# Performance work log

Measured on AMD Instinct MI355X. Metric: run time of the kernel, lower is better.

The kernel has to match this reference:

```python
import jax, jax.numpy as jnp
import numpy as np

H = 512      # cfg.hidden_size
I = 512      # input_size
T = 64       # cfg.recurrence
B = 1024     # num_trajectories

def setup_inputs() -> dict:
    key = jax.random.key(0)
    ks = jax.random.split(key, 7)
    s = 1.0 / np.sqrt(H)
    head_output = jax.random.normal(ks[0], (B * T, I), jnp.float32)
    rnn_states = jax.random.normal(ks[1], (B, 2 * H), jnp.float32)
    dones = jax.random.randint(ks[2], (B * T,), 0, 2).astype(jnp.float32)
    W_ih = jax.random.uniform(ks[3], (4 * H, I), jnp.float32, -s, s)
    W_hh = jax.random.uniform(ks[4], (4 * H, H), jnp.float32, -s, s)
    b_ih = jax.random.uniform(ks[5], (4 * H,), jnp.float32, -s, s)
    b_hh = jax.random.uniform(ks[6], (4 * H,), jnp.float32, -s, s)
    return {"head_output": head_output, "rnn_states": rnn_states, "dones": dones,
            "W_ih": W_ih, "W_hh": W_hh, "b_ih": b_ih, "b_hh": b_hh}

def reference(head_output, rnn_states, dones, W_ih, W_hh, b_ih, b_hh):
    # h, c: [B, H] each (num_layers == 1)
    h0, c0 = jnp.split(rnn_states, 2, axis=1)
    x_seq = head_output.reshape(B, T, I).transpose(1, 0, 2)  # [T, B, I]
    # is_new_episode = dones rolled by 1 along time, first step forced to 0
    d = dones.reshape(B, T)
    is_new = jnp.roll(d, 1, axis=1).at[:, 0].set(0.0)  # [B, T]
    masks = is_new.T  # [T, B]
    # precompute input projection for all steps (same math, hoisted out of the loop)
    x_proj = jnp.einsum('tbi,gi->tbg', x_seq, W_ih) + b_ih + b_hh  # [T, B, 4H]

    def step(carry, inp):
        h, c = carry
        xp, m = inp
        keep = (1.0 - m)[:, None]  # zero state at episode boundaries
        h = h * keep
        c = c * keep
        gates = xp + h @ W_hh.T  # [B, 4H], torch gate order i,f,g,o
        i_g, f_g, g_g, o_g = jnp.split(gates, 4, axis=1)
        i_g = jax.nn.sigmoid(i_g)
        f_g = jax.nn.sigmoid(f_g)
        g_g = jnp.tanh(g_g)
        o_g = jax.nn.sigmoid(o_g)
        c = f_g * c + i_g * g_g
        h = o_g * jnp.tanh(c)
        return (h, c), (h, c)

    (hT, cT), (hs, cs) = jax.lax.scan(step, (h0, c0), (x_proj, masks))
    # outputs at each step are h (output of single-layer LSTM)
    x = hs.transpose(1, 0, 2).reshape(B * T, H)  # [B*T, H]
    new_rnn_states = jnp.concatenate((hT, cT), axis=1)  # [B, 2H]
    h_stack = hs[:, None, :, :]  # [T, 1, B, H] (num_layers dim)
    c_stack = cs[:, None, :, :]
    return x, new_rnn_states, (h_stack, c_stack)
```

## Files before the change

kernel.cpp:

```cpp
#include <hip/hip_runtime.h>
#include <stdint.h>


#define WC_OFF   0u
#define HF_OFF   4194304u
#define CF_OFF   5242880u
#define BIAS_OFF 7340032u
#define F_WIH   0u
#define F_WHH   2097152u
#define F_HF    4194304u
#define F_CF    5242880u
#define F_BIAS  7340032u
#define F_XBF   8388608u
#define F_XPROJ 75497472u
#define F_NEED  343932928u
#define OUT_RNN  33554432u
#define OUT_HS   34603008u
#define OUT_CS   68157440u

typedef __attribute__((ext_vector_type(4))) float f32x4;
typedef __attribute__((ext_vector_type(8))) short s16x8;
typedef __attribute__((ext_vector_type(4))) unsigned int u32x4;
typedef __attribute__((ext_vector_type(4))) unsigned short u16x4;

__device__ __forceinline__ unsigned short f2bf(float f) {
  union { float f; unsigned int u; } v; v.f = f;
  return (unsigned short)((v.u + 0x7FFFu + ((v.u >> 16) & 1u)) >> 16);
}
__device__ __forceinline__ float bf2f(unsigned short s) {
  union { unsigned int u; float f; } v; v.u = ((unsigned int)s) << 16;
  return v.f;
}
__device__ __forceinline__ unsigned int pack2(float a, float b) {
  return (unsigned int)f2bf(a) | ((unsigned int)f2bf(b) << 16);
}
__device__ __forceinline__ float sigm(float x) { return 1.0f / (1.0f + __expf(-x)); }

__device__ __forceinline__ void gl_lds16(const void* g, void* lds) {
  __builtin_amdgcn_global_load_lds(
      (const __attribute__((address_space(1))) unsigned int*)g,
      (__attribute__((address_space(3))) unsigned int*)lds, 16, 0, 0);
}



__global__ void __launch_bounds__(256) prep_fast(
    const float* __restrict__ xg, const float* __restrict__ rnn,
    const float* __restrict__ Wih, const float* __restrict__ Whh,
    const float* __restrict__ bih, const float* __restrict__ bhh,
    unsigned char* __restrict__ ws) {
  unsigned int tid = blockIdx.x * 256u + threadIdx.x;
  unsigned short* wih_f = (unsigned short*)(ws + F_WIH);
  unsigned short* whh_f = (unsigned short*)(ws + F_WHH);
  unsigned short* hf    = (unsigned short*)(ws + F_HF);
  float* cf   = (float*)(ws + F_CF);
  float* bias = (float*)(ws + F_BIAS);
  unsigned short* xbf = (unsigned short*)(ws + F_XBF);
  if (tid < 131072u) {
    unsigned int frag = tid >> 6, l = tid & 63u;
    unsigned int cb = frag >> 4, ks = frag & 15u;
    unsigned int g  = cb * 16u + (l & 15u);
    unsigned int k0 = ks * 32u + ((l >> 4) << 3);
    const float* src = Wih + (size_t)g * 512u + k0;
    u32x4 p;
    p.x = pack2(src[0], src[1]); p.y = pack2(src[2], src[3]);
    p.z = pack2(src[4], src[5]); p.w = pack2(src[6], src[7]);
    *(u32x4*)(wih_f + (size_t)frag * 512u + l * 8u) = p;
  } else if (tid < 262144u) {
    unsigned int t2 = tid - 131072u;
    unsigned int frag = t2 >> 6, l = t2 & 63u;
    unsigned int cb = frag >> 4, ks = frag & 15u;
    unsigned int g  = cb * 16u + (l & 15u);
    unsigned int k0 = ks * 32u + ((l >> 4) << 3);
    const float* src = Whh + (size_t)g * 512u + k0;
    u32x4 p;
    p.x = pack2(src[0], src[1]); p.y = pack2(src[2], src[3]);
    p.z = pack2(src[4], src[5]); p.w = pack2(src[6], src[7]);
    *(u32x4*)(whh_f + (size_t)frag * 512u + l * 8u) = p;
  } else if (tid < 327680u) {
    unsigned int t2 = tid - 262144u;
    unsigned int frag = t2 >> 6, l = t2 & 63u;
    unsigned int mb = frag >> 4, ks = frag & 15u;
    unsigned int b  = mb * 16u + (l & 15u);
    unsigned int c0 = ks * 32u + ((l >> 4) << 3);
    const float* src = rnn + (size_t)b * 1024u + c0;
    u32x4 p;
    p.x = pack2(src[0], src[1]); p.y = pack2(src[2], src[3]);
    p.z = pack2(src[4], src[5]); p.w = pack2(src[6], src[7]);
    *(u32x4*)(hf + (size_t)frag * 512u + l * 8u) = p;
  } else if (tid < 458752u) {
    unsigned int t2 = tid - 327680u;
    unsigned int frag = t2 >> 6, l = t2 & 63u;
    unsigned int mb = frag >> 5, cfi = frag & 31u;
    unsigned int hcol = cfi * 16u + (l & 15u);
    f32x4 p;
    #pragma unroll
    for (int r = 0; r < 4; ++r) {
      unsigned int b = mb * 16u + ((l >> 4) << 2) + r;
      p[r] = rnn[(size_t)b * 1024u + 512u + hcol];
    }
    *(f32x4*)(cf + (size_t)frag * 256u + l * 4u) = p;
  } else if (tid < 460800u) {
    unsigned int g = tid - 458752u;
    bias[g] = bih[g] + bhh[g];
  } else if (tid < 4655104u) {
    unsigned int t2 = tid - 460800u;
    unsigned int frag = t2 >> 6, l = t2 & 63u;
    unsigned int ks = frag & 15u, mb = (frag >> 4) & 63u, t = frag >> 10;
    unsigned int b  = mb * 16u + (l & 15u);
    unsigned int k0 = ks * 32u + ((l >> 4) << 3);
    const float* src = xg + ((size_t)(b * 64u + t)) * 512u + k0;
    u32x4 p;
    p.x = pack2(src[0], src[1]); p.y = pack2(src[2], src[3]);
    p.z = pack2(src[4], src[5]); p.w = pack2(src[6], src[7]);
    *(u32x4*)(xbf + (size_t)frag * 512u + l * 8u) = p;
  }
}

__global__ void __launch_bounds__(256) gemm_xproj(unsigned char* __restrict__ ws) {
  const unsigned short* xbf = (const unsigned short*)(ws + F_XBF);
  const unsigned short* wih = (const unsigned short*)(ws + F_WIH);
  const float* bias = (const float*)(ws + F_BIAS);
  unsigned short* xproj = (unsigned short*)(ws + F_XPROJ);

  __shared__ __align__(16) unsigned char smem[65536];
  const int tid = threadIdx.x;
  const int w = tid >> 6, l = tid & 63;
  const int mh = w & 1, nh = w >> 1;
  const int bid = blockIdx.x;
  const int t = bid >> 7, mtile = (bid >> 4) & 7, ntile = bid & 15;

  f32x4 acc[4][4];
  {
    f32x4 z = {0.f, 0.f, 0.f, 0.f};
    #pragma unroll
    for (int i = 0; i < 4; ++i)
      #pragma unroll
      for (int j = 0; j < 4; ++j) acc[i][j] = z;
  }

  auto stage = [&](int kc, int buf) {
    unsigned char* ab = smem + buf * 16384;
    unsigned char* bb = smem + 32768 + buf * 16384;
    #pragma unroll
    for (int j = 0; j < 4; ++j) {
      int idx = w * 4 + j;
      int mb_l = idx >> 1, ksl = idx & 1;
      size_t frag = (size_t)(t * 64 + mtile * 8 + mb_l) * 16u + kc * 2 + ksl;
      gl_lds16(xbf + (frag * 64u + l) * 8u, ab + idx * 1024);
    }
    #pragma unroll
    for (int j = 0; j < 4; ++j) {
      int idx = w * 4 + j;
      int cb_l = idx >> 1, ksl = idx & 1;
      size_t frag = (size_t)(ntile * 8 + cb_l) * 16u + kc * 2 + ksl;
      gl_lds16(wih + (frag * 64u + l) * 8u, bb + idx * 1024);
    }
  };

  stage(0, 0);
  __syncthreads();
  for (int kc = 0; kc < 8; ++kc) {
    int cur = kc & 1;
    if (kc < 7) stage(kc + 1, cur ^ 1);
    unsigned char* ab = smem + cur * 16384;
    unsigned char* bb = smem + 32768 + cur * 16384;
    s16x8 afr[4][2], bfr[4][2];
    #pragma unroll
    for (int m = 0; m < 4; ++m)
      #pragma unroll
      for (int ksl = 0; ksl < 2; ++ksl)
        afr[m][ksl] = *(const s16x8*)(ab + ((mh * 4 + m) * 2 + ksl) * 1024 + l * 16);
    #pragma unroll
    for (int n = 0; n < 4; ++n)
      #pragma unroll
      for (int ksl = 0; ksl < 2; ++ksl)
        bfr[n][ksl] = *(const s16x8*)(bb + ((nh * 4 + n) * 2 + ksl) * 1024 + l * 16);
    #pragma unroll
    for (int m = 0; m < 4; ++m)
      #pragma unroll
      for (int n = 0; n < 4; ++n)
        #pragma unroll
        for (int ksl = 0; ksl < 2; ++ksl)
          acc[m][n] = __builtin_amdgcn_mfma_f32_16x16x32_bf16(
              afr[m][ksl], bfr[n][ksl], acc[m][n], 0, 0, 0);
    __syncthreads();
  }

  #pragma unroll
  for (int m = 0; m < 4; ++m) {
    int mb_abs = mtile * 8 + mh * 4 + m;
    #pragma unroll
    for (int n = 0; n < 4; ++n) {
      int n_abs = ntile * 8 + nh * 4 + n;
      float bc = bias[n_abs * 16 + (l & 15)];
      u16x4 p;
      #pragma unroll
      for (int r = 0; r < 4; ++r) p[r] = f2bf(acc[m][n][r] + bc);
      *(u16x4*)(xproj + ((size_t)(t * 64 + mb_abs) * 128u + n_abs) * 256u + l * 4u) = p;
    }
  }
}

__global__ void __launch_bounds__(256) step_fast(
    const float* __restrict__ dones, unsigned char* __restrict__ ws,
    float* __restrict__ out, int t) {
  const unsigned short* whh = (const unsigned short*)(ws + F_WHH);
  unsigned short* hf = (unsigned short*)(ws + F_HF);
  float* cf = (float*)(ws + F_CF);
  const unsigned short* xproj = (const unsigned short*)(ws + F_XPROJ);

  __shared__ __align__(16) unsigned char smem[49152];
  const int tid = threadIdx.x;
  const int w = tid >> 6, l = tid & 63;
  const int mh = w & 1, ch = w >> 1;
  const int mt = (int)blockIdx.x >> 4, ht = (int)blockIdx.x & 15;

  f32x4 acc[2][4];
  {
    f32x4 z = {0.f, 0.f, 0.f, 0.f};
    #pragma unroll
    for (int i = 0; i < 2; ++i)
      #pragma unroll
      for (int j = 0; j < 4; ++j) acc[i][j] = z;
  }

  auto stage = [&](int kc, int buf) {
    unsigned char* bb = smem + 16384 + buf * 16384;
    #pragma unroll
    for (int j = 0; j < 4; ++j) {
      int idx = w * 4 + j;
      int g = idx >> 2, cbl = (idx >> 1) & 1, ksl = idx & 1;
      int cb = g * 32 + ht * 2 + cbl;
      int ks = kc * 2 + ksl;
      gl_lds16(whh + ((size_t)(cb * 16 + ks) * 64u + l) * 8u, bb + idx * 1024);
    }
    unsigned char* ab = smem + buf * 8192;
    #pragma unroll
    for (int j = 0; j < 2; ++j) {
      int idx = w * 2 + j;
      int mb_l = idx >> 1, ksl = idx & 1;
      int frag = (mt * 4 + mb_l) * 16 + kc * 2 + ksl;
      gl_lds16(hf + ((size_t)frag * 64u + l) * 8u, ab + idx * 1024);
    }
  };

  stage(0, 0);
  __syncthreads();
  for (int kc = 0; kc < 8; ++kc) {
    int cur = kc & 1;
    if (kc < 7) stage(kc + 1, cur ^ 1);
    unsigned char* ab = smem + cur * 8192;
    unsigned char* bb = smem + 16384 + cur * 16384;
    s16x8 afr[2][2], bfr[4][2];
    #pragma unroll
    for (int mb2 = 0; mb2 < 2; ++mb2)
      #pragma unroll
      for (int ksl = 0; ksl < 2; ++ksl)
        afr[mb2][ksl] = *(const s16x8*)(ab + ((mh * 2 + mb2) * 2 + ksl) * 1024 + l * 16);
    #pragma unroll
    for (int g = 0; g < 4; ++g)
      #pragma unroll
      for (int ksl = 0; ksl < 2; ++ksl)
        bfr[g][ksl] = *(const s16x8*)(bb + (g * 4 + ch * 2 + ksl) * 1024 + l * 16);
    #pragma unroll
    for (int mb2 = 0; mb2 < 2; ++mb2)
      #pragma unroll
      for (int g = 0; g < 4; ++g)
        #pragma unroll
        for (int ksl = 0; ksl < 2; ++ksl)
          acc[mb2][g] = __builtin_amdgcn_mfma_f32_16x16x32_bf16(
              afr[mb2][ksl], bfr[g][ksl], acc[mb2][g], 0, 0, 0);
    __syncthreads();
  }

  #pragma unroll
  for (int mb2 = 0; mb2 < 2; ++mb2) {
    int mb_abs = mt * 4 + mh * 2 + mb2;
    #pragma unroll
    for (int g = 0; g < 4; ++g) {
      int n_abs = g * 32 + ht * 2 + ch;
      u16x4 xpv = *(const u16x4*)(xproj + ((size_t)(t * 64 + mb_abs) * 128u + n_abs) * 256u + l * 4u);
      #pragma unroll
      for (int r = 0; r < 4; ++r) acc[mb2][g][r] += bf2f(xpv[r]);
    }
  }

  float* Hl = (float*)smem;
  float* Cl = (float*)(smem + 9216);
  const int cfi = ht * 2 + ch;
  const int colL = ch * 16 + (l & 15);
  #pragma unroll
  for (int mb2 = 0; mb2 < 2; ++mb2) {
    const int mb_abs = mt * 4 + mh * 2 + mb2;
    const int fid = mb_abs * 32 + cfi;
    f32x4 cold = *(const f32x4*)(cf + (size_t)fid * 256u + l * 4u);
    f32x4 cmask;
    #pragma unroll
    for (int r = 0; r < 4; ++r) {
      float gi = sigm(acc[mb2][0][r]);
      float gf = sigm(acc[mb2][1][r]);
      float gg = tanhf(acc[mb2][2][r]);
      float go = sigm(acc[mb2][3][r]);
      float c = gf * cold[r] + gi * gg;
      float h = go * tanhf(c);
      int brow = mb_abs * 16 + ((l >> 4) << 2) + r;
      float keep = 1.0f - dones[brow * 64 + t];
      cmask[r] = c * keep;
      int rowL = mh * 32 + mb2 * 16 + ((l >> 4) << 2) + r;
      Hl[rowL * 36 + colL] = h;
      Cl[rowL * 36 + colL] = c;
    }
    *(f32x4*)(cf + (size_t)fid * 256u + l * 4u) = cmask;
  }
  __syncthreads();

  {
    const int mb2f = tid >> 6, lp = tid & 63;
    const int mb_abs = mt * 4 + mb2f;
    const int rowL = mb2f * 16 + (lp & 15);
    const int c0 = (lp >> 4) << 3;
    const int brow = mt * 64 + rowL;
    const float keep = 1.0f - dones[brow * 64 + t];
    const float* hr = Hl + rowL * 36 + c0;
    u32x4 p;
    p.x = pack2(hr[0] * keep, hr[1] * keep);
    p.y = pack2(hr[2] * keep, hr[3] * keep);
    p.z = pack2(hr[4] * keep, hr[5] * keep);
    p.w = pack2(hr[6] * keep, hr[7] * keep);
    *(u32x4*)(hf + ((size_t)(mb_abs * 16 + ht) * 64u + lp) * 8u) = p;
  }
  {
    const int row = tid & 63, cg = tid >> 6;
    const int b = mt * 64 + row;
    const int c0 = cg * 8;
    const float* hr = Hl + row * 36 + c0;
    const float* cr = Cl + row * 36 + c0;
    f32x4 h0 = *(const f32x4*)hr,  h1 = *(const f32x4*)(hr + 4);
    f32x4 cc0 = *(const f32x4*)cr, cc1 = *(const f32x4*)(cr + 4);
    const int colg = ht * 32 + c0;
    size_t xoff = ((size_t)(b * 64 + t)) * 512u + colg;
    *(f32x4*)(out + xoff) = h0; *(f32x4*)(out + xoff + 4) = h1;
    size_t hoff = OUT_HS + ((size_t)(t * 1024 + b)) * 512u + colg;
    *(f32x4*)(out + hoff) = h0; *(f32x4*)(out + hoff + 4) = h1;
    size_t coff = OUT_CS + ((size_t)(t * 1024 + b)) * 512u + colg;
    *(f32x4*)(out + coff) = cc0; *(f32x4*)(out + coff + 4) = cc1;
    if (t == 63) {
      size_t roff = OUT_RNN + (size_t)b * 1024u + colg;
      *(f32x4*)(out + roff) = h0;        *(f32x4*)(out + roff + 4) = h1;
      *(f32x4*)(out + roff + 512) = cc0; *(f32x4*)(out + roff + 516) = cc1;
    }
  }
}


__global__ void __launch_bounds__(256) prep_kernel(
    const float* __restrict__ rnn, const float* __restrict__ Wih,
    const float* __restrict__ Whh, const float* __restrict__ bih,
    const float* __restrict__ bhh, unsigned char* __restrict__ ws) {
  unsigned int tid = blockIdx.x * 256u + threadIdx.x;
  unsigned short* wcf = (unsigned short*)(ws + WC_OFF);
  unsigned short* hf  = (unsigned short*)(ws + HF_OFF);
  float* cf   = (float*)(ws + CF_OFF);
  float* bias = (float*)(ws + BIAS_OFF);
  if (tid < 262144u) {
    unsigned int frag = tid >> 6, l = tid & 63u;
    unsigned int cb = frag >> 5, ks = frag & 31u;
    unsigned int g  = cb * 16u + (l & 15u);
    unsigned int k0 = ks * 32u + ((l >> 4) << 3);
    const float* src = (k0 < 512u) ? (Wih + g * 512u + k0) : (Whh + g * 512u + (k0 - 512u));
    u32x4 p;
    p.x = pack2(src[0], src[1]); p.y = pack2(src[2], src[3]);
    p.z = pack2(src[4], src[5]); p.w = pack2(src[6], src[7]);
    *(u32x4*)(wcf + (size_t)frag * 512u + l * 8u) = p;
  } else if (tid < 327680u) {
    unsigned int t2 = tid - 262144u;
    unsigned int frag = t2 >> 6, l = t2 & 63u;
    unsigned int mb = frag >> 4, ks = frag & 15u;
    unsigned int b  = mb * 16u + (l & 15u);
    unsigned int c0 = ks * 32u + ((l >> 4) << 3);
    const float* src = rnn + (size_t)b * 1024u + c0;
    u32x4 p;
    p.x = pack2(src[0], src[1]); p.y = pack2(src[2], src[3]);
    p.z = pack2(src[4], src[5]); p.w = pack2(src[6], src[7]);
    *(u32x4*)(hf + (size_t)frag * 512u + l * 8u) = p;
  } else if (tid < 458752u) {
    unsigned int t2 = tid - 327680u;
    unsigned int frag = t2 >> 6, l = t2 & 63u;
    unsigned int mb = frag >> 5, cfi = frag & 31u;
    unsigned int hcol = cfi * 16u + (l & 15u);
    f32x4 p;
    #pragma unroll
    for (int r = 0; r < 4; ++r) {
      unsigned int b = mb * 16u + ((l >> 4) << 2) + r;
      p[r] = rnn[(size_t)b * 1024u + 512u + hcol];
    }
    *(f32x4*)(cf + (size_t)frag * 256u + l * 4u) = p;
  } else if (tid < 460800u) {
    unsigned int g = tid - 458752u;
    bias[g] = bih[g] + bhh[g];
  }
}

__global__ void __launch_bounds__(256) step_kernel(
    const float* __restrict__ xg, const float* __restrict__ dones,
    unsigned char* __restrict__ ws, float* __restrict__ out, int t) {
  const unsigned short* wcf = (const unsigned short*)(ws + WC_OFF);
  unsigned short* hf = (unsigned short*)(ws + HF_OFF);
  float* cf = (float*)(ws + CF_OFF);
  const float* bias = (const float*)(ws + BIAS_OFF);

  __shared__ __align__(16) unsigned char smem[49152];
  const int tid = threadIdx.x;
  const int w = tid >> 6, l = tid & 63;
  const int mh = w & 1, ch = w >> 1;
  const int mt = (int)blockIdx.x >> 4, ht = (int)blockIdx.x & 15;

  f32x4 acc[2][4];
  {
    f32x4 z = {0.f, 0.f, 0.f, 0.f};
    #pragma unroll
    for (int i = 0; i < 2; ++i)
      #pragma unroll
      for (int j = 0; j < 4; ++j) acc[i][j] = z;
  }

  f32x4 xv[2][2];

  auto stage_load = [&](int kc, int buf) {
    unsigned char* bb = smem + 16384 + buf * 16384;
    #pragma unroll
    for (int j = 0; j < 4; ++j) {
      int idx = w * 4 + j;
      int g = idx >> 2, cbl = (idx >> 1) & 1, ksl = idx & 1;
      int cb = g * 32 + ht * 2 + cbl;
      int ks = kc * 2 + ksl;
      const unsigned short* src = wcf + ((size_t)(cb * 32 + ks) * 64u + l) * 8u;
      gl_lds16(src, bb + idx * 1024);
    }
    unsigned char* ab = smem + buf * 8192;
    if (kc >= 8) {
      #pragma unroll
      for (int j = 0; j < 2; ++j) {
        int idx = w * 2 + j;
        int ksh = (kc - 8) * 2 + j;
        int mb_abs = mt * 4 + w;
        const unsigned short* src = hf + ((size_t)(mb_abs * 16 + ksh) * 64u + l) * 8u;
        gl_lds16(src, ab + idx * 1024);
      }
    } else {
      #pragma unroll
      for (int j = 0; j < 2; ++j) {
        int ks = kc * 2 + j;
        int b = mt * 64 + w * 16 + (l & 15);
        int k0 = ks * 32 + ((l >> 4) << 3);
        const float* src = xg + ((size_t)(b * 64 + t)) * 512u + k0;
        xv[j][0] = *(const f32x4*)src;
        xv[j][1] = *(const f32x4*)(src + 4);
      }
    }
  };
  auto stage_write = [&](int kc, int buf) {
    if (kc < 8) {
      unsigned char* ab = smem + buf * 8192;
      #pragma unroll
      for (int j = 0; j < 2; ++j) {
        int idx = w * 2 + j;
        u32x4 p;
        p.x = pack2(xv[j][0].x, xv[j][0].y); p.y = pack2(xv[j][0].z, xv[j][0].w);
        p.z = pack2(xv[j][1].x, xv[j][1].y); p.w = pack2(xv[j][1].z, xv[j][1].w);
        *(u32x4*)(ab + idx * 1024 + l * 16) = p;
      }
    }
  };

  stage_load(0, 0);
  stage_write(0, 0);
  __syncthreads();

  for (int kc = 0; kc < 16; ++kc) {
    int cur = kc & 1;
    if (kc < 15) stage_load(kc + 1, cur ^ 1);
    unsigned char* ab = smem + cur * 8192;
    unsigned char* bb = smem + 16384 + cur * 16384;
    s16x8 afr[2][2], bfr[4][2];
    #pragma unroll
    for (int mb2 = 0; mb2 < 2; ++mb2)
      #pragma unroll
      for (int ksl = 0; ksl < 2; ++ksl)
        afr[mb2][ksl] = *(const s16x8*)(ab + ((mh * 2 + mb2) * 2 + ksl) * 1024 + l * 16);
    #pragma unroll
    for (int g = 0; g < 4; ++g)
      #pragma unroll
      for (int ksl = 0; ksl < 2; ++ksl)
        bfr[g][ksl] = *(const s16x8*)(bb + (g * 4 + ch * 2 + ksl) * 1024 + l * 16);
    #pragma unroll
    for (int mb2 = 0; mb2 < 2; ++mb2)
      #pragma unroll
      for (int g = 0; g < 4; ++g)
        #pragma unroll
        for (int ksl = 0; ksl < 2; ++ksl)
          acc[mb2][g] = __builtin_amdgcn_mfma_f32_16x16x32_bf16(
              afr[mb2][ksl], bfr[g][ksl], acc[mb2][g], 0, 0, 0);
    if (kc < 15) stage_write(kc + 1, cur ^ 1);
    __syncthreads();
  }

  const int hcol = ht * 32 + ch * 16 + (l & 15);
  const float bi = bias[hcol], bf2 = bias[512 + hcol];
  const float bg = bias[1024 + hcol], bo = bias[1536 + hcol];
  float* Hl = (float*)smem;
  float* Cl = (float*)(smem + 9216);
  const int cfi = ht * 2 + ch;
  const int colL = ch * 16 + (l & 15);
  #pragma unroll
  for (int mb2 = 0; mb2 < 2; ++mb2) {
    const int mb_abs = mt * 4 + mh * 2 + mb2;
    const int fid = mb_abs * 32 + cfi;
    f32x4 cold = *(const f32x4*)(cf + (size_t)fid * 256u + l * 4u);
    f32x4 cmask;
    #pragma unroll
    for (int r = 0; r < 4; ++r) {
      float gi = sigm(acc[mb2][0][r] + bi);
      float gf = sigm(acc[mb2][1][r] + bf2);
      float gg = tanhf(acc[mb2][2][r] + bg);
      float go = sigm(acc[mb2][3][r] + bo);
      float c = gf * cold[r] + gi * gg;
      float h = go * tanhf(c);
      int brow = mb_abs * 16 + ((l >> 4) << 2) + r;
      float keep = 1.0f - dones[brow * 64 + t];
      cmask[r] = c * keep;
      int rowL = mh * 32 + mb2 * 16 + ((l >> 4) << 2) + r;
      Hl[rowL * 36 + colL] = h;
      Cl[rowL * 36 + colL] = c;
    }
    *(f32x4*)(cf + (size_t)fid * 256u + l * 4u) = cmask;
  }
  __syncthreads();

  {
    const int mb2f = tid >> 6, lp = tid & 63;
    const int mb_abs = mt * 4 + mb2f;
    const int rowL = mb2f * 16 + (lp & 15);
    const int c0 = (lp >> 4) << 3;
    const int brow = mt * 64 + rowL;
    const float keep = 1.0f - dones[brow * 64 + t];
    const float* hr = Hl + rowL * 36 + c0;
    u32x4 p;
    p.x = pack2(hr[0] * keep, hr[1] * keep);
    p.y = pack2(hr[2] * keep, hr[3] * keep);
    p.z = pack2(hr[4] * keep, hr[5] * keep);
    p.w = pack2(hr[6] * keep, hr[7] * keep);
    *(u32x4*)(hf + ((size_t)(mb_abs * 16 + ht) * 64u + lp) * 8u) = p;
  }
  {
    const int row = tid & 63, cg = tid >> 6;
    const int b = mt * 64 + row;
    const int c0 = cg * 8;
    const float* hr = Hl + row * 36 + c0;
    const float* cr = Cl + row * 36 + c0;
    f32x4 h0 = *(const f32x4*)hr,  h1 = *(const f32x4*)(hr + 4);
    f32x4 cc0 = *(const f32x4*)cr, cc1 = *(const f32x4*)(cr + 4);
    const int colg = ht * 32 + c0;
    size_t xoff = ((size_t)(b * 64 + t)) * 512u + colg;
    *(f32x4*)(out + xoff) = h0; *(f32x4*)(out + xoff + 4) = h1;
    size_t hoff = OUT_HS + ((size_t)(t * 1024 + b)) * 512u + colg;
    *(f32x4*)(out + hoff) = h0; *(f32x4*)(out + hoff + 4) = h1;
    size_t coff = OUT_CS + ((size_t)(t * 1024 + b)) * 512u + colg;
    *(f32x4*)(out + coff) = cc0; *(f32x4*)(out + coff + 4) = cc1;
    if (t == 63) {
      size_t roff = OUT_RNN + (size_t)b * 1024u + colg;
      *(f32x4*)(out + roff) = h0;        *(f32x4*)(out + roff + 4) = h1;
      *(f32x4*)(out + roff + 512) = cc0; *(f32x4*)(out + roff + 516) = cc1;
    }
  }
}

extern "C" void kernel_launch(void* const* d_in, const int* in_sizes, int n_in,
                              void* d_out, int out_size, void* d_ws, size_t ws_size,
                              hipStream_t stream) {
  const float* xg  = (const float*)d_in[0];
  const float* rnn = (const float*)d_in[1];
  const float* dn  = (const float*)d_in[2];
  const float* Wih = (const float*)d_in[3];
  const float* Whh = (const float*)d_in[4];
  const float* bih = (const float*)d_in[5];
  const float* bhh = (const float*)d_in[6];
  float* out = (float*)d_out;
  unsigned char* ws = (unsigned char*)d_ws;
  (void)in_sizes; (void)n_in; (void)out_size;

  if (ws_size >= (size_t)F_NEED) {
    prep_fast<<<18184, 256, 0, stream>>>(xg, rnn, Wih, Whh, bih, bhh, ws);
    gemm_xproj<<<8192, 256, 0, stream>>>(ws);
    for (int t = 0; t < 64; ++t)
      step_fast<<<256, 256, 0, stream>>>(dn, ws, out, t);
  } else {
    prep_kernel<<<1800, 256, 0, stream>>>(rnn, Wih, Whh, bih, bhh, ws);
    for (int t = 0; t < 64; ++t)
      step_kernel<<<256, 256, 0, stream>>>(xg, dn, ws, out, t);
  }
}
```

Before: 1.143 ms.

## Load full W_hh slice to LDS once and keep h fragments in registers

```diff
diff --git a/kernel.cpp b/kernel.cpp
--- a/kernel.cpp
+++ b/kernel.cpp
@@ -202,7 +202,7 @@
   }
 }
 
-__global__ void __launch_bounds__(256) step_fast(
+__global__ void __launch_bounds__(256, 1) step_fast(
     const float* __restrict__ dones, unsigned char* __restrict__ ws,
     float* __restrict__ out, int t) {
   const unsigned short* whh = (const unsigned short*)(ws + F_WHH);
@@ -210,12 +210,51 @@
   float* cf = (float*)(ws + F_CF);
   const unsigned short* xproj = (const unsigned short*)(ws + F_XPROJ);
 
-  __shared__ __align__(16) unsigned char smem[49152];
+  __shared__ __align__(16) unsigned char smem[131072];
   const int tid = threadIdx.x;
   const int w = tid >> 6, l = tid & 63;
   const int mh = w & 1, ch = w >> 1;
   const int mt = (int)blockIdx.x >> 4, ht = (int)blockIdx.x & 15;
 
+  #pragma unroll
+  for (int j = 0; j < 32; ++j) {
+    int idx = w * 32 + j;
+    int gcb = idx >> 4, ks = idx & 15;
+    int cb = (gcb >> 1) * 32 + ht * 2 + (gcb & 1);
+    gl_lds16(whh + ((size_t)(cb * 16 + ks) * 64u + l) * 8u, smem + idx * 1024);
+  }
+
+  s16x8 areg[2][16];
+  #pragma unroll
+  for (int mb2 = 0; mb2 < 2; ++mb2) {
+    int frag0 = (mt * 4 + mh * 2 + mb2) * 16;
+    #pragma unroll
+    for (int ks = 0; ks < 16; ++ks)
+      areg[mb2][ks] = *(const s16x8*)(hf + ((size_t)(frag0 + ks) * 64u + l) * 8u);
+  }
+
+  u16x4 xpv[2][4];
+  f32x4 cold[2];
+  f32x4 kv[2];
+  const int cfi = ht * 2 + ch;
+  #pragma unroll
+  for (int mb2 = 0; mb2 < 2; ++mb2) {
+    const int mb_abs = mt * 4 + mh * 2 + mb2;
+    #pragma unroll
+    for (int g = 0; g < 4; ++g) {
+      int n_abs = g * 32 + ht * 2 + ch;
+      xpv[mb2][g] = *(const u16x4*)(xproj +
+          ((size_t)(t * 64 + mb_abs) * 128u + n_abs) * 256u + l * 4u);
+    }
+    cold[mb2] = *(const f32x4*)(cf + (size_t)(mb_abs * 32 + cfi) * 256u + l * 4u);
+    #pragma unroll
+    for (int r = 0; r < 4; ++r) {
+      int brow = mb_abs * 16 + ((l >> 4) << 2) + r;
+      kv[mb2][r] = dones[brow * 64 + t];
+    }
+  }
+  const float keep2 = 1.0f - dones[(mt * 64 + (tid >> 6) * 16 + (tid & 15)) * 64 + t];
+
   f32x4 acc[2][4];
   {
     f32x4 z = {0.f, 0.f, 0.f, 0.f};
@@ -225,44 +264,17 @@
       for (int j = 0; j < 4; ++j) acc[i][j] = z;
   }
 
-  auto stage = [&](int kc, int buf) {
-    unsigned char* bb = smem + 16384 + buf * 16384;
-    #pragma unroll
-    for (int j = 0; j < 4; ++j) {
-      int idx = w * 4 + j;
-      int g = idx >> 2, cbl = (idx >> 1) & 1, ksl = idx & 1;
-      int cb = g * 32 + ht * 2 + cbl;
-      int ks = kc * 2 + ksl;
-      gl_lds16(whh + ((size_t)(cb * 16 + ks) * 64u + l) * 8u, bb + idx * 1024);
-    }
-    unsigned char* ab = smem + buf * 8192;
-    #pragma unroll
-    for (int j = 0; j < 2; ++j) {
-      int idx = w * 2 + j;
-      int mb_l = idx >> 1, ksl = idx & 1;
-      int frag = (mt * 4 + mb_l) * 16 + kc * 2 + ksl;
-      gl_lds16(hf + ((size_t)frag * 64u + l) * 8u, ab + idx * 1024);
-    }
-  };
-
-  stage(0, 0);
   __syncthreads();
+
+  #pragma unroll
   for (int kc = 0; kc < 8; ++kc) {
-    int cur = kc & 1;
-    if (kc < 7) stage(kc + 1, cur ^ 1);
-    unsigned char* ab = smem + cur * 8192;
-    unsigned char* bb = smem + 16384 + cur * 16384;
-    s16x8 afr[2][2], bfr[4][2];
-    #pragma unroll
-    for (int mb2 = 0; mb2 < 2; ++mb2)
+    s16x8 bfr[4][2];
+    #pragma unroll
+    for (int g = 0; g < 4; ++g)
       #pragma unroll
       for (int ksl = 0; ksl < 2; ++ksl)
-        afr[mb2][ksl] = *(const s16x8*)(ab + ((mh * 2 + mb2) * 2 + ksl) * 1024 + l * 16);
-    #pragma unroll
-    for (int g = 0; g < 4; ++g)
-      #pragma unroll
-      for (int ksl = 0; ksl < 2; ++ksl)
-        bfr[g][ksl] = *(const s16x8*)(bb + (g * 4 + ch * 2 + ksl) * 1024 + l * 16);
+        bfr[g][ksl] = *(const s16x8*)(smem +
+            (((g * 2 + ch) * 16) + kc * 2 + ksl) * 1024 + l * 16);
     #pragma unroll
     for (int mb2 = 0; mb2 < 2; ++mb2)
       #pragma unroll
@@ -270,31 +282,26 @@
         #pragma unroll
         for (int ksl = 0; ksl < 2; ++ksl)
           acc[mb2][g] = __builtin_amdgcn_mfma_f32_16x16x32_bf16(
-              afr[mb2][ksl], bfr[g][ksl], acc[mb2][g], 0, 0, 0);
-    __syncthreads();
-  }
-
-  #pragma unroll
-  for (int mb2 = 0; mb2 < 2; ++mb2) {
-    int mb_abs = mt * 4 + mh * 2 + mb2;
-    #pragma unroll
-    for (int g = 0; g < 4; ++g) {
-      int n_abs = g * 32 + ht * 2 + ch;
-      u16x4 xpv = *(const u16x4*)(xproj + ((size_t)(t * 64 + mb_abs) * 128u + n_abs) * 256u + l * 4u);
-      #pragma unroll
-      for (int r = 0; r < 4; ++r) acc[mb2][g][r] += bf2f(xpv[r]);
-    }
-  }
+              areg[mb2][kc * 2 + ksl], bfr[g][ksl], acc[mb2][g], 0, 0, 0);
+  }
+
+  #pragma unroll
+  for (int mb2 = 0; mb2 < 2; ++mb2)
+    #pragma unroll
+    for (int g = 0; g < 4; ++g)
+      #pragma unroll
+      for (int r = 0; r < 4; ++r)
+        acc[mb2][g][r] += bf2f(xpv[mb2][g][r]);
+
+  __syncthreads();
 
   float* Hl = (float*)smem;
   float* Cl = (float*)(smem + 9216);
-  const int cfi = ht * 2 + ch;
   const int colL = ch * 16 + (l & 15);
   #pragma unroll
   for (int mb2 = 0; mb2 < 2; ++mb2) {
     const int mb_abs = mt * 4 + mh * 2 + mb2;
     const int fid = mb_abs * 32 + cfi;
-    f32x4 cold = *(const f32x4*)(cf + (size_t)fid * 256u + l * 4u);
     f32x4 cmask;
     #pragma unroll
     for (int r = 0; r < 4; ++r) {
@@ -302,10 +309,9 @@
       float gf = sigm(acc[mb2][1][r]);
       float gg = tanhf(acc[mb2][2][r]);
       float go = sigm(acc[mb2][3][r]);
-      float c = gf * cold[r] + gi * gg;
+      float c = gf * cold[mb2][r] + gi * gg;
       float h = go * tanhf(c);
-      int brow = mb_abs * 16 + ((l >> 4) << 2) + r;
-      float keep = 1.0f - dones[brow * 64 + t];
+      float keep = 1.0f - kv[mb2][r];
       cmask[r] = c * keep;
       int rowL = mh * 32 + mb2 * 16 + ((l >> 4) << 2) + r;
       Hl[rowL * 36 + colL] = h;
@@ -320,14 +326,12 @@
     const int mb_abs = mt * 4 + mb2f;
     const int rowL = mb2f * 16 + (lp & 15);
     const int c0 = (lp >> 4) << 3;
-    const int brow = mt * 64 + rowL;
-    const float keep = 1.0f - dones[brow * 64 + t];
     const float* hr = Hl + rowL * 36 + c0;
     u32x4 p;
-    p.x = pack2(hr[0] * keep, hr[1] * keep);
-    p.y = pack2(hr[2] * keep, hr[3] * keep);
-    p.z = pack2(hr[4] * keep, hr[5] * keep);
-    p.w = pack2(hr[6] * keep, hr[7] * keep);
+    p.x = pack2(hr[0] * keep2, hr[1] * keep2);
+    p.y = pack2(hr[2] * keep2, hr[3] * keep2);
+    p.z = pack2(hr[4] * keep2, hr[5] * keep2);
+    p.w = pack2(hr[6] * keep2, hr[7] * keep2);
     *(u32x4*)(hf + ((size_t)(mb_abs * 16 + ht) * 64u + lp) * 8u) = p;
   }
   {
```

After: 1.030 ms. 9.9% less time.
